# Optimization experiments

Measured on AMD Instinct MI355X. Metric: run time of the kernel, lower is better.

The kernel has to match this reference:

```python
import jax, jax.numpy as jnp
import numpy as np

K = 3
BN_EPS = 1e-3


def setup_inputs() -> dict:
    key = jax.random.key(0)
    ks = jax.random.split(key, 13)
    B, N1, N2 = 8, 1024, 4096
    C1, C2, Cs = 256, 128, 64
    Ctot = C1 + C2 + Cs  # 448
    H = 256
    return {
        "points1": jax.random.normal(ks[0], (B, 3, N1), jnp.float32),
        "points2": jax.random.normal(ks[1], (B, 3, N2), jnp.float32),
        "features1": jax.random.normal(ks[2], (B, C1, N1), jnp.float32),
        "features2": jax.random.normal(ks[3], (B, C2, N2), jnp.float32),
        "skip_features": jax.random.normal(ks[4], (B, Cs, N2), jnp.float32),
        # 1x1 Conv2d weights are equivalent to dense matrices [out, in]
        "W1": jax.random.normal(ks[5], (H, Ctot), jnp.float32) * 0.05,
        "b1": jax.random.normal(ks[6], (H,), jnp.float32) * 0.05,
        "g1": 1.0 + jax.random.normal(ks[7], (H,), jnp.float32) * 0.05,
        "beta1": jax.random.normal(ks[8], (H,), jnp.float32) * 0.05,
        "W2": jax.random.normal(ks[9], (H, H), jnp.float32) * 0.05,
        "b2": jax.random.normal(ks[10], (H,), jnp.float32) * 0.05,
        "g2": 1.0 + jax.random.normal(ks[11], (H,), jnp.float32) * 0.05,
        "beta2": jax.random.normal(ks[12], (H,), jnp.float32) * 0.05,
    }


def _conv_bn_relu(x, W, b, g, beta):
    # x: [B, N, Cin]; 1x1 conv == dense matmul per point
    y = jnp.einsum("bnc,oc->bno", x, W) + b
    # BatchNorm2d in training mode: batch stats over (batch, spatial) per channel
    mu = jnp.mean(y, axis=(0, 1))
    var = jnp.mean(jnp.square(y - mu), axis=(0, 1))  # biased variance
    y = (y - mu) * jax.lax.rsqrt(var + BN_EPS) * g + beta
    return jax.nn.relu(y)


def reference(points1, points2, features1, features2, skip_features,
              W1, b1, g1, beta1, W2, b2, g2, beta2):
    p1 = jnp.swapaxes(points1, 1, 2)  # [B, N1, 3]
    p2 = jnp.swapaxes(points2, 1, 2)  # [B, N2, 3]
    # pairwise Euclidean distances [B, N2, N1]
    d2 = (jnp.sum(p2 * p2, -1, keepdims=True)
          + jnp.sum(p1 * p1, -1)[:, None, :]
          - 2.0 * jnp.einsum("bnd,bmd->bnm", p2, p1))
    dist = jnp.sqrt(jnp.maximum(d2, 0.0))
    # k smallest distances
    neg_top, ind = jax.lax.top_k(-dist, K)  # ind: [B, N2, K]
    dk = -neg_top
    inv = 1.0 / (dk + 1e-10)
    w = inv / jnp.sum(inv, -1, keepdims=True)  # [B, N2, K]
    f1 = jnp.swapaxes(features1, 1, 2)  # [B, N1, C1]
    gathered = jax.vmap(lambda f, i: f[i])(f1, ind)  # [B, N2, K, C1]
    new = jnp.einsum("bnkc,bnk->bnc", gathered, w)  # inverse-distance interp
    x = jnp.concatenate([new,
                         jnp.swapaxes(features2, 1, 2),
                         jnp.swapaxes(skip_features, 1, 2)], axis=-1)
    x = _conv_bn_relu(x, W1, b1, g1, beta1)
    x = _conv_bn_relu(x, W2, b2, g2, beta2)
    return jnp.swapaxes(x, 1, 2)  # [B, Cout, N2]
```

## Files before the change

kernel.cpp:

```cpp
#include <hip/hip_runtime.h>
#include <cstdint>
#include <cstddef>

#define B_    8
#define N1_   1024
#define N2_   4096
#define C1_   256
#define C2_   128
#define CS_   64
#define CT_   448
#define H_    256
#define ROWS_ (B_ * N2_)

typedef __attribute__((ext_vector_type(8))) short bf16x8;
typedef __attribute__((ext_vector_type(4))) float f32x4;
typedef unsigned short ushort_t;
typedef unsigned int   uint_t;

__device__ __forceinline__ ushort_t f2bf(float f) {
    uint_t u = __float_as_uint(f);
    u = (u + 0x7fffu + ((u >> 16) & 1u)) >> 16;
    return (ushort_t)u;
}
__device__ __forceinline__ float bf2f(ushort_t h) {
    return __uint_as_float(((uint_t)h) << 16);
}

__global__ __launch_bounds__(256) void knn_kernel(
    const float* __restrict__ p1, const float* __restrict__ p2,
    int* __restrict__ ind, float* __restrict__ wout)
{
#pragma clang fp contract(off)
    __shared__ float4 cand[N1_ + 8];
    __shared__ float  pdd[16][32][3];
    __shared__ int    pdi[16][32][3];
    __shared__ float  pdd2[4][32][3];
    __shared__ int    pdi2[4][32][3];
    const int t = threadIdx.x;
    const int b  = blockIdx.x >> 7;
    const int qb = (blockIdx.x & 127) * 32;
    const float* pb1 = p1 + (size_t)b * 3 * N1_;
    for (int i = t; i < N1_; i += 256) {
        float X = pb1[i], Y = pb1[N1_ + i], Z = pb1[2 * N1_ + i];
        cand[i] = make_float4(X, Y, Z, (X * X + Y * Y) + Z * Z);
    }
    const int qp = t & 15, split = t >> 4;
    const int na = qb + 2 * qp, nb = na + 1;
    const float* pb2 = p2 + (size_t)b * 3 * N2_;
    const float ax = pb2[na], ay = pb2[N2_ + na], az = pb2[2 * N2_ + na];
    const float bx = pb2[nb], by = pb2[N2_ + nb], bz = pb2[2 * N2_ + nb];
    const float s2a = (ax * ax + ay * ay) + az * az;
    const float s2b = (bx * bx + by * by) + bz * bz;
    __syncthreads();
    float a0 = 3e38f, a1 = 3e38f, a2 = 3e38f;  int ai0 = 0, ai1 = 0, ai2 = 0;
    float b0 = 3e38f, b1 = 3e38f, b2 = 3e38f;  int bi0 = 0, bi1 = 0, bi2 = 0;
    const int ibeg = split * 64;
    float4 c = cand[ibeg];
    for (int i = ibeg; i < ibeg + 64; ++i) {
        float4 cn = cand[i + 1];
        float dota = (ax * c.x + ay * c.y) + az * c.z;
        float dda  = (s2a + c.w) - 2.0f * dota;
        float da   = sqrtf(fmaxf(dda, 0.0f));
        float dotb = (bx * c.x + by * c.y) + bz * c.z;
        float ddb  = (s2b + c.w) - 2.0f * dotb;
        float db   = sqrtf(fmaxf(ddb, 0.0f));
        if (da < a0)      { a2 = a1; ai2 = ai1; a1 = a0; ai1 = ai0; a0 = da; ai0 = i; }
        else if (da < a1) { a2 = a1; ai2 = ai1; a1 = da; ai1 = i; }
        else if (da < a2) { a2 = da; ai2 = i; }
        if (db < b0)      { b2 = b1; bi2 = bi1; b1 = b0; bi1 = bi0; b0 = db; bi0 = i; }
        else if (db < b1) { b2 = b1; bi2 = bi1; b1 = db; bi1 = i; }
        else if (db < b2) { b2 = db; bi2 = i; }
        c = cn;
    }
    const int qa = 2 * qp, qbq = 2 * qp + 1;
    pdd[split][qa][0] = a0;  pdd[split][qa][1] = a1;  pdd[split][qa][2] = a2;
    pdi[split][qa][0] = ai0; pdi[split][qa][1] = ai1; pdi[split][qa][2] = ai2;
    pdd[split][qbq][0] = b0;  pdd[split][qbq][1] = b1;  pdd[split][qbq][2] = b2;
    pdi[split][qbq][0] = bi0; pdi[split][qbq][1] = bi1; pdi[split][qbq][2] = bi2;
    __syncthreads();
    if (t < 128) {
        const int q = t & 31, g = t >> 5;
        float e0 = 3e38f, e1 = 3e38f, e2 = 3e38f;
        int   j0 = 0, j1 = 0, j2 = 0;
#pragma unroll
        for (int s = 0; s < 4; ++s) {
            const int sp = g * 4 + s;
#pragma unroll
            for (int r = 0; r < 3; ++r) {
                float d = pdd[sp][q][r];
                int   i = pdi[sp][q][r];
                if (d < e0)      { e2 = e1; j2 = j1; e1 = e0; j1 = j0; e0 = d; j0 = i; }
                else if (d < e1) { e2 = e1; j2 = j1; e1 = d;  j1 = i; }
                else if (d < e2) { e2 = d;  j2 = i; }
            }
        }
        pdd2[g][q][0] = e0; pdd2[g][q][1] = e1; pdd2[g][q][2] = e2;
        pdi2[g][q][0] = j0; pdi2[g][q][1] = j1; pdi2[g][q][2] = j2;
    }
    __syncthreads();
    if (t < 32) {
        float e0 = 3e38f, e1 = 3e38f, e2 = 3e38f;
        int   j0 = 0, j1 = 0, j2 = 0;
#pragma unroll
        for (int g = 0; g < 4; ++g) {
#pragma unroll
            for (int r = 0; r < 3; ++r) {
                float d = pdd2[g][t][r];
                int   i = pdi2[g][t][r];
                if (d < e0)      { e2 = e1; j2 = j1; e1 = e0; j1 = j0; e0 = d; j0 = i; }
                else if (d < e1) { e2 = e1; j2 = j1; e1 = d;  j1 = i; }
                else if (d < e2) { e2 = d;  j2 = i; }
            }
        }
        float inv0 = 1.0f / (e0 + 1e-10f);
        float inv1 = 1.0f / (e1 + 1e-10f);
        float inv2 = 1.0f / (e2 + 1e-10f);
        float s = (inv0 + inv1) + inv2;
        const size_t row = (size_t)b * N2_ + qb + t;
        wout[row * 3 + 0] = inv0 / s;
        wout[row * 3 + 1] = inv1 / s;
        wout[row * 3 + 2] = inv2 / s;
        ind[row * 3 + 0] = j0;
        ind[row * 3 + 1] = j1;
        ind[row * 3 + 2] = j2;
    }
}

__global__ __launch_bounds__(256) void prep_kernel(
    const float* __restrict__ f1, const float* __restrict__ f2,
    const float* __restrict__ fs, const float* __restrict__ W1,
    const float* __restrict__ W2, ushort_t* __restrict__ f1t,
    ushort_t* __restrict__ x, ushort_t* __restrict__ W1b, ushort_t* __restrict__ W2b)
{
    __shared__ float tile[64][65];
    const int t = threadIdx.x;
    const int bid0 = blockIdx.x;
    if (bid0 < 512) {
        const int bid = bid0;
        const int b  = bid >> 6;
        const int ct = (bid >> 4) & 3;
        const int nt = bid & 15;
        const int c0 = ct * 64, n0 = nt * 64;
        const float* src = f1 + ((size_t)b * C1_ + c0) * N1_ + n0;
#pragma unroll
        for (int j = 0; j < 16; ++j) {
            int lin = j * 256 + t;
            int ci = lin >> 6, nj = lin & 63;
            tile[ci][nj] = src[(size_t)ci * N1_ + nj];
        }
        __syncthreads();
        ushort_t* dst = f1t + ((size_t)b * N1_ + n0) * C1_ + c0;
#pragma unroll
        for (int j = 0; j < 8; ++j) {
            int lin = j * 256 + t;
            int ni = lin >> 5, cjp = (lin & 31) * 2;
            uint_t u = (uint_t)f2bf(tile[cjp][ni]) | ((uint_t)f2bf(tile[cjp + 1][ni]) << 16);
            *(uint_t*)&dst[(size_t)ni * C1_ + cjp] = u;
        }
    } else if (bid0 < 2048) {
        const int bid = bid0 - 512;
        const int b   = bid / 192;
        const int rem = bid - b * 192;
        const int ct  = rem >> 6;
        const int nt  = rem & 63;
        const float* src;
        int coff;
        if (ct < 2) { src = f2 + ((size_t)b * C2_ + ct * 64) * N2_; coff = C1_ + ct * 64; }
        else        { src = fs + (size_t)b * CS_ * N2_;             coff = C1_ + C2_; }
        const int n0 = nt * 64;
#pragma unroll
        for (int j = 0; j < 16; ++j) {
            int lin = j * 256 + t;
            int ci = lin >> 6, nj = lin & 63;
            tile[ci][nj] = src[(size_t)ci * N2_ + n0 + nj];
        }
        __syncthreads();
#pragma unroll
        for (int j = 0; j < 8; ++j) {
            int lin = j * 256 + t;
            int ni = lin >> 5, cjp = (lin & 31) * 2;
            uint_t u = (uint_t)f2bf(tile[cjp][ni]) | ((uint_t)f2bf(tile[cjp + 1][ni]) << 16);
            *(uint_t*)&x[((size_t)b * N2_ + n0 + ni) * CT_ + coff + cjp] = u;
        }
    } else {
        const int i = (bid0 - 2048) * 256 + t;
        if (i < H_ * CT_) W1b[i] = f2bf(W1[i]);
        if (i < H_ * H_)  W2b[i] = f2bf(W2[i]);
    }
}

__global__ __launch_bounds__(256) void gather_x(
    const ushort_t* __restrict__ f1t, const int* __restrict__ ind,
    const float* __restrict__ w, ushort_t* __restrict__ x)
{
    const int t = threadIdx.x;
    const int row = blockIdx.x * 8 + (t >> 5);
    const int b = row >> 12;
    const int cg = (t & 31) * 8;
    const int*   ip = ind + (size_t)row * 3;
    const float* wp = w   + (size_t)row * 3;
    const int i0 = ip[0], i1 = ip[1], i2 = ip[2];
    const float w0 = wp[0], w1 = wp[1], w2 = wp[2];
    const ushort_t* base = f1t + (size_t)b * N1_ * C1_;
    uint4 va = *(const uint4*)(base + (size_t)i0 * C1_ + cg);
    uint4 vb = *(const uint4*)(base + (size_t)i1 * C1_ + cg);
    uint4 vc = *(const uint4*)(base + (size_t)i2 * C1_ + cg);
    const uint_t* pa = (const uint_t*)&va;
    const uint_t* pb = (const uint_t*)&vb;
    const uint_t* pc = (const uint_t*)&vc;
    uint_t out[4];
#pragma unroll
    for (int e = 0; e < 4; ++e) {
        float lo = w0 * bf2f((ushort_t)(pa[e] & 0xffff))
                 + w1 * bf2f((ushort_t)(pb[e] & 0xffff))
                 + w2 * bf2f((ushort_t)(pc[e] & 0xffff));
        float hi = w0 * bf2f((ushort_t)(pa[e] >> 16))
                 + w1 * bf2f((ushort_t)(pb[e] >> 16))
                 + w2 * bf2f((ushort_t)(pc[e] >> 16));
        out[e] = (uint_t)f2bf(lo) | ((uint_t)f2bf(hi) << 16);
    }
    *(uint4*)&x[(size_t)row * CT_ + cg] = *(uint4*)out;
}

__global__ __launch_bounds__(256, 4) void gemm_bf16(
    const ushort_t* __restrict__ A, const ushort_t* __restrict__ Bw,
    const float* __restrict__ bias, ushort_t* __restrict__ C,
    float* __restrict__ ssum, float* __restrict__ ssq, int K)
{
    __shared__ __align__(16) ushort_t smem[128 * 72];
    ushort_t* As = smem;
    ushort_t* Bs = smem + 5120;
    ushort_t* Cs = smem;
    const int t = threadIdx.x;
    const int m0 = blockIdx.x * 128;
    const int n0 = blockIdx.y * 64;
    const int lane = t & 63;
    const int wv = t >> 6;
    const int wrow = wv & 1, wcol = wv >> 1;
    const int lm = lane & 15, lq = lane >> 4;
    const int crow = t >> 2, ckc = (t & 3) * 8;
    f32x4 acc[4][2];
#pragma unroll
    for (int i = 0; i < 4; ++i)
#pragma unroll
        for (int j = 0; j < 2; ++j)
            acc[i][j] = (f32x4){0.f, 0.f, 0.f, 0.f};

    for (int k0 = 0; k0 < K; k0 += 32) {
        uint4 a0 = *(const uint4*)(A  + (size_t)(m0 + crow) * K + k0 + ckc);
        uint4 a1 = *(const uint4*)(A  + (size_t)(m0 + 64 + crow) * K + k0 + ckc);
        uint4 b0 = *(const uint4*)(Bw + (size_t)(n0 + crow) * K + k0 + ckc);
        __syncthreads();
        *(uint4*)&As[crow * 40 + ckc]        = a0;
        *(uint4*)&As[(64 + crow) * 40 + ckc] = a1;
        *(uint4*)&Bs[crow * 40 + ckc]        = b0;
        __syncthreads();
        bf16x8 af[4], bfr[2];
#pragma unroll
        for (int i = 0; i < 4; ++i)
            af[i] = *(const bf16x8*)&As[(wrow * 64 + i * 16 + lm) * 40 + lq * 8];
#pragma unroll
        for (int j = 0; j < 2; ++j)
            bfr[j] = *(const bf16x8*)&Bs[(wcol * 32 + j * 16 + lm) * 40 + lq * 8];
#pragma unroll
        for (int i = 0; i < 4; ++i)
#pragma unroll
            for (int j = 0; j < 2; ++j)
                acc[i][j] = __builtin_amdgcn_mfma_f32_16x16x32_bf16(af[i], bfr[j], acc[i][j], 0, 0, 0);
    }
    __syncthreads();
#pragma unroll
    for (int j = 0; j < 2; ++j) {
        const int gn_l = wcol * 32 + j * 16 + lm;
        const int gn   = n0 + gn_l;
        const float bb = bias[gn];
        float ps = 0.0f, pq = 0.0f;
#pragma unroll
        for (int i = 0; i < 4; ++i) {
            const int row_l = wrow * 64 + i * 16 + lq * 4;
            f32x4 v = acc[i][j];
#pragma unroll
            for (int r = 0; r < 4; ++r) {
                float val = v[r] + bb;
                ps += val;
                pq += val * val;
                float vo = __shfl_xor(val, 1);
                uint_t packed = (lm & 1)
                    ? ((uint_t)f2bf(vo)  | ((uint_t)f2bf(val) << 16))
                    : ((uint_t)f2bf(val) | ((uint_t)f2bf(vo)  << 16));
                if ((lm & 1) == 0)
                    *(uint_t*)&Cs[(row_l + r) * 72 + (gn_l & ~1)] = packed;
            }
        }
        ps += __shfl_xor(ps, 16); pq += __shfl_xor(pq, 16);
        ps += __shfl_xor(ps, 32); pq += __shfl_xor(pq, 32);
        if (lane < 16) {
            atomicAdd(&ssum[gn], ps);
            atomicAdd(&ssq[gn], pq);
        }
    }
    __syncthreads();
    const int srow = t >> 3;
    const int scol = (t & 7) * 8;
#pragma unroll
    for (int rep = 0; rep < 4; ++rep) {
        const int row = srow + rep * 32;
        uint4 v = *(const uint4*)&Cs[row * 72 + scol];
        *(uint4*)(C + (size_t)(m0 + row) * H_ + n0 + scol) = v;
    }
}

__global__ __launch_bounds__(256) void bn_relu_mid(
    const ushort_t* __restrict__ y, const float* __restrict__ ssum,
    const float* __restrict__ ssq, const float* __restrict__ g,
    const float* __restrict__ beta, ushort_t* __restrict__ yn)
{
    __shared__ float sc[H_], sh[H_];
    const int t = threadIdx.x;
    {
        const float invN = 1.0f / (float)ROWS_;
        float mu  = ssum[t] * invN;
        float var = ssq[t] * invN - mu * mu;
        float s   = rsqrtf(var + 1e-3f) * g[t];
        sc[t] = s;
        sh[t] = beta[t] - mu * s;
    }
    __syncthreads();
    const int c0 = (t & 31) * 8;
    float s[8], h[8];
#pragma unroll
    for (int e = 0; e < 8; ++e) { s[e] = sc[c0 + e]; h[e] = sh[c0 + e]; }
    const uint4* yin = (const uint4*)y;
    uint4* yout = (uint4*)yn;
    const size_t base = (size_t)blockIdx.x * 4096 + t;
#pragma unroll
    for (int j = 0; j < 16; ++j) {
        uint4 u = yin[base + j * 256];
        uint_t* uw = (uint_t*)&u;
        uint_t o[4];
#pragma unroll
        for (int e = 0; e < 4; ++e) {
            float lo = __uint_as_float(uw[e] << 16);
            float hi = __uint_as_float(uw[e] & 0xffff0000u);
            float rlo = fmaxf(fmaf(lo, s[2 * e],     h[2 * e]),     0.0f);
            float rhi = fmaxf(fmaf(hi, s[2 * e + 1], h[2 * e + 1]), 0.0f);
            o[e] = (uint_t)f2bf(rlo) | ((uint_t)f2bf(rhi) << 16);
        }
        yout[base + j * 256] = *(uint4*)o;
    }
}

__global__ __launch_bounds__(256) void bn_out_kernel(
    const ushort_t* __restrict__ y, const float* __restrict__ ssum, const float* __restrict__ ssq,
    const float* __restrict__ g, const float* __restrict__ beta, float* __restrict__ out)
{
    __shared__ float tile[64][65];
    __shared__ float sc[64], sh[64];
    const float invN = 1.0f / (float)ROWS_;
    const int bid = blockIdx.x;
    const int b  = bid >> 8;
    const int nt = (bid >> 2) & 63;
    const int ot = bid & 3;
    const int t = threadIdx.x;
    if (t < 64) {
        int c = ot * 64 + t;
        float mu  = ssum[c] * invN;
        float var = ssq[c] * invN - mu * mu;
        float s   = rsqrtf(var + 1e-3f) * g[c];
        sc[t] = s;
        sh[t] = beta[c] - mu * s;
    }
    __syncthreads();
    const int n0 = nt * 64, o0 = ot * 64;
    const ushort_t* yb = y + ((size_t)b * N2_ + n0) * H_ + o0;
#pragma unroll
    for (int j = 0; j < 8; ++j) {
        int lin = j * 256 + t;
        int nl = lin >> 5, cu = (lin & 31) * 2;
        uint_t u = *(const uint_t*)&yb[(size_t)nl * H_ + cu];
        tile[nl][cu]     = fmaxf(bf2f((ushort_t)(u & 0xffff)) * sc[cu]     + sh[cu],     0.0f);
        tile[nl][cu + 1] = fmaxf(bf2f((ushort_t)(u >> 16))    * sc[cu + 1] + sh[cu + 1], 0.0f);
    }
    __syncthreads();
    float* ob = out + ((size_t)b * H_ + o0) * N2_ + n0;
#pragma unroll
    for (int j = 0; j < 16; ++j) {
        int lin = j * 256 + t;
        int ol = lin >> 6, nl = lin & 63;
        ob[(size_t)ol * N2_ + nl] = tile[nl][ol];
    }
}

extern "C" void kernel_launch(void* const* d_in, const int* in_sizes, int n_in,
                              void* d_out, int out_size, void* d_ws, size_t ws_size,
                              hipStream_t stream)
{
    (void)in_sizes; (void)n_in; (void)out_size; (void)ws_size;
    const float* points1   = (const float*)d_in[0];
    const float* points2   = (const float*)d_in[1];
    const float* features1 = (const float*)d_in[2];
    const float* features2 = (const float*)d_in[3];
    const float* skipf     = (const float*)d_in[4];
    const float* W1  = (const float*)d_in[5];
    const float* b1  = (const float*)d_in[6];
    const float* g1  = (const float*)d_in[7];
    const float* be1 = (const float*)d_in[8];
    const float* W2  = (const float*)d_in[9];
    const float* b2  = (const float*)d_in[10];
    const float* g2  = (const float*)d_in[11];
    const float* be2 = (const float*)d_in[12];
    float* out = (float*)d_out;

    char* ws = (char*)d_ws;
    float*    s1  = (float*)(ws + 0);
    float*    q1  = (float*)(ws + 1024);
    float*    s2  = (float*)(ws + 2048);
    float*    q2  = (float*)(ws + 3072);
    int*      ind = (int*)(ws + 4096);
    float*    wgt = (float*)(ws + 397312);
    ushort_t* x   = (ushort_t*)(ws + 790528);
    ushort_t* y1b = (ushort_t*)(ws + 30150656);
    ushort_t* y1n = (ushort_t*)(ws + 46927872);
    ushort_t* W1b = (ushort_t*)(ws + 63705088);
    ushort_t* W2b = (ushort_t*)(ws + 63934464);
    ushort_t* f1t = (ushort_t*)(ws + 64065536);
    ushort_t* y2b = x;

    hipMemsetAsync(ws, 0, 4096, stream);

    knn_kernel<<<dim3(1024), dim3(256), 0, stream>>>(points1, points2, ind, wgt);
    prep_kernel<<<dim3(2496), dim3(256), 0, stream>>>(features1, features2, skipf,
                                                      W1, W2, f1t, x, W1b, W2b);
    gather_x<<<dim3(4096), dim3(256), 0, stream>>>(f1t, ind, wgt, x);

    gemm_bf16<<<dim3(ROWS_ / 128, 4), dim3(256), 0, stream>>>(x, W1b, b1, y1b, s1, q1, CT_);
    bn_relu_mid<<<dim3(256), dim3(256), 0, stream>>>(y1b, s1, q1, g1, be1, y1n);
    gemm_bf16<<<dim3(ROWS_ / 128, 4), dim3(256), 0, stream>>>(y1n, W2b, b2, y2b, s2, q2, H_);
    bn_out_kernel<<<dim3(2048), dim3(256), 0, stream>>>(y2b, s2, q2, g2, be2, out);
}
```

Before: 236.1 us.

## Fuse KNN into prep kernel and use threshold-pruned two-pass top-3 search

Merges the KNN and prep kernels into a single launch whose block ranges do distinct jobs, sharing one dynamic-layout LDS buffer. The KNN part now handles one query per thread over a quarter of the candidates. A first pass tracks the top-3 squared distances with fmin/fmed3 and no sqrt or branching, then derives a per-query threshold. A second pass collects up to 12 candidates under that threshold and runs exact sqrt-based top-3 on only those. This removes per-candidate sqrt and branchy insertion and saves a launch, but it repeats the distance scan and the fixed 12-entry cap with a 2e-3 margin could drop true neighbours in rare dense cases.

Measured after the change: 215.1 us. 8.9% less time.

```diff
diff --git a/kernel.cpp b/kernel.cpp
--- a/kernel.cpp
+++ b/kernel.cpp
@@ -26,120 +26,123 @@
     return __uint_as_float(((uint_t)h) << 16);
 }
 
-__global__ __launch_bounds__(256) void knn_kernel(
+__global__ __launch_bounds__(256) void fused_pre(
     const float* __restrict__ p1, const float* __restrict__ p2,
-    int* __restrict__ ind, float* __restrict__ wout)
-{
-#pragma clang fp contract(off)
-    __shared__ float4 cand[N1_ + 8];
-    __shared__ float  pdd[16][32][3];
-    __shared__ int    pdi[16][32][3];
-    __shared__ float  pdd2[4][32][3];
-    __shared__ int    pdi2[4][32][3];
-    const int t = threadIdx.x;
-    const int b  = blockIdx.x >> 7;
-    const int qb = (blockIdx.x & 127) * 32;
-    const float* pb1 = p1 + (size_t)b * 3 * N1_;
-    for (int i = t; i < N1_; i += 256) {
-        float X = pb1[i], Y = pb1[N1_ + i], Z = pb1[2 * N1_ + i];
-        cand[i] = make_float4(X, Y, Z, (X * X + Y * Y) + Z * Z);
-    }
-    const int qp = t & 15, split = t >> 4;
-    const int na = qb + 2 * qp, nb = na + 1;
-    const float* pb2 = p2 + (size_t)b * 3 * N2_;
-    const float ax = pb2[na], ay = pb2[N2_ + na], az = pb2[2 * N2_ + na];
-    const float bx = pb2[nb], by = pb2[N2_ + nb], bz = pb2[2 * N2_ + nb];
-    const float s2a = (ax * ax + ay * ay) + az * az;
-    const float s2b = (bx * bx + by * by) + bz * bz;
-    __syncthreads();
-    float a0 = 3e38f, a1 = 3e38f, a2 = 3e38f;  int ai0 = 0, ai1 = 0, ai2 = 0;
-    float b0 = 3e38f, b1 = 3e38f, b2 = 3e38f;  int bi0 = 0, bi1 = 0, bi2 = 0;
-    const int ibeg = split * 64;
-    float4 c = cand[ibeg];
-    for (int i = ibeg; i < ibeg + 64; ++i) {
-        float4 cn = cand[i + 1];
-        float dota = (ax * c.x + ay * c.y) + az * c.z;
-        float dda  = (s2a + c.w) - 2.0f * dota;
-        float da   = sqrtf(fmaxf(dda, 0.0f));
-        float dotb = (bx * c.x + by * c.y) + bz * c.z;
-        float ddb  = (s2b + c.w) - 2.0f * dotb;
-        float db   = sqrtf(fmaxf(ddb, 0.0f));
-        if (da < a0)      { a2 = a1; ai2 = ai1; a1 = a0; ai1 = ai0; a0 = da; ai0 = i; }
-        else if (da < a1) { a2 = a1; ai2 = ai1; a1 = da; ai1 = i; }
-        else if (da < a2) { a2 = da; ai2 = i; }
-        if (db < b0)      { b2 = b1; bi2 = bi1; b1 = b0; bi1 = bi0; b0 = db; bi0 = i; }
-        else if (db < b1) { b2 = b1; bi2 = bi1; b1 = db; bi1 = i; }
-        else if (db < b2) { b2 = db; bi2 = i; }
-        c = cn;
-    }
-    const int qa = 2 * qp, qbq = 2 * qp + 1;
-    pdd[split][qa][0] = a0;  pdd[split][qa][1] = a1;  pdd[split][qa][2] = a2;
-    pdi[split][qa][0] = ai0; pdi[split][qa][1] = ai1; pdi[split][qa][2] = ai2;
-    pdd[split][qbq][0] = b0;  pdd[split][qbq][1] = b1;  pdd[split][qbq][2] = b2;
-    pdi[split][qbq][0] = bi0; pdi[split][qbq][1] = bi1; pdi[split][qbq][2] = bi2;
-    __syncthreads();
-    if (t < 128) {
-        const int q = t & 31, g = t >> 5;
-        float e0 = 3e38f, e1 = 3e38f, e2 = 3e38f;
-        int   j0 = 0, j1 = 0, j2 = 0;
-#pragma unroll
-        for (int s = 0; s < 4; ++s) {
-            const int sp = g * 4 + s;
-#pragma unroll
-            for (int r = 0; r < 3; ++r) {
-                float d = pdd[sp][q][r];
-                int   i = pdi[sp][q][r];
-                if (d < e0)      { e2 = e1; j2 = j1; e1 = e0; j1 = j0; e0 = d; j0 = i; }
-                else if (d < e1) { e2 = e1; j2 = j1; e1 = d;  j1 = i; }
-                else if (d < e2) { e2 = d;  j2 = i; }
-            }
-        }
-        pdd2[g][q][0] = e0; pdd2[g][q][1] = e1; pdd2[g][q][2] = e2;
-        pdi2[g][q][0] = j0; pdi2[g][q][1] = j1; pdi2[g][q][2] = j2;
-    }
-    __syncthreads();
-    if (t < 32) {
-        float e0 = 3e38f, e1 = 3e38f, e2 = 3e38f;
-        int   j0 = 0, j1 = 0, j2 = 0;
-#pragma unroll
-        for (int g = 0; g < 4; ++g) {
-#pragma unroll
-            for (int r = 0; r < 3; ++r) {
-                float d = pdd2[g][t][r];
-                int   i = pdi2[g][t][r];
-                if (d < e0)      { e2 = e1; j2 = j1; e1 = e0; j1 = j0; e0 = d; j0 = i; }
-                else if (d < e1) { e2 = e1; j2 = j1; e1 = d;  j1 = i; }
-                else if (d < e2) { e2 = d;  j2 = i; }
-            }
-        }
-        float inv0 = 1.0f / (e0 + 1e-10f);
-        float inv1 = 1.0f / (e1 + 1e-10f);
-        float inv2 = 1.0f / (e2 + 1e-10f);
-        float s = (inv0 + inv1) + inv2;
-        const size_t row = (size_t)b * N2_ + qb + t;
-        wout[row * 3 + 0] = inv0 / s;
-        wout[row * 3 + 1] = inv1 / s;
-        wout[row * 3 + 2] = inv2 / s;
-        ind[row * 3 + 0] = j0;
-        ind[row * 3 + 1] = j1;
-        ind[row * 3 + 2] = j2;
-    }
-}
-
-__global__ __launch_bounds__(256) void prep_kernel(
+    int* __restrict__ ind, float* __restrict__ wout,
     const float* __restrict__ f1, const float* __restrict__ f2,
     const float* __restrict__ fs, const float* __restrict__ W1,
     const float* __restrict__ W2, ushort_t* __restrict__ f1t,
     ushort_t* __restrict__ x, ushort_t* __restrict__ W1b, ushort_t* __restrict__ W2b)
 {
-    __shared__ float tile[64][65];
+#pragma clang fp contract(off)
+    __shared__ __align__(16) char smem[32000];
     const int t = threadIdx.x;
-    const int bid0 = blockIdx.x;
-    if (bid0 < 512) {
-        const int bid = bid0;
+    const int bid = blockIdx.x;
+    if (bid < 512) {
+        float4*   cand  = (float4*)(smem);
+        float*    pvals = (float*)(smem + 16384);
+        float*    thr   = (float*)(smem + 19456);
+        ushort_t* lists = (ushort_t*)(smem + 19712);
+        float*    pdd   = (float*)(smem + 25856);
+        int*      pdi   = (int*)(smem + 28928);
         const int b  = bid >> 6;
-        const int ct = (bid >> 4) & 3;
-        const int nt = bid & 15;
+        const int qb = (bid & 63) * 64;
+        const float* pb1 = p1 + (size_t)b * 3 * N1_;
+        for (int i = t; i < N1_; i += 256) {
+            float X = pb1[i], Y = pb1[N1_ + i], Z = pb1[2 * N1_ + i];
+            cand[i] = make_float4(X, Y, Z, (X * X + Y * Y) + Z * Z);
+        }
+        const int q = t & 63, quarter = t >> 6;
+        const int n = qb + q;
+        const float* pb2 = p2 + (size_t)b * 3 * N2_;
+        const float ax = pb2[n], ay = pb2[N2_ + n], az = pb2[2 * N2_ + n];
+        const float s2a = (ax * ax + ay * ay) + az * az;
+        const float m2x = -2.0f * ax, m2y = -2.0f * ay, m2z = -2.0f * az;
+        __syncthreads();
+        const int ibeg = quarter * 256, iend = ibeg + 256;
+        {
+            float a0 = 3e38f, a1 = 3e38f, a2 = 3e38f;
+            for (int i = ibeg; i < iend; ++i) {
+                float4 c = cand[i];
+                float fd = fmaf(c.x, m2x, fmaf(c.y, m2y, fmaf(c.z, m2z, s2a + c.w)));
+                float o0 = a0, o1 = a1;
+                a0 = fminf(o0, fd);
+                a1 = __builtin_amdgcn_fmed3f(fd, o0, o1);
+                a2 = __builtin_amdgcn_fmed3f(fd, o1, a2);
+            }
+            pvals[t * 3 + 0] = a0; pvals[t * 3 + 1] = a1; pvals[t * 3 + 2] = a2;
+        }
+        __syncthreads();
+        if (t < 64) {
+            float m0 = 3e38f, m1 = 3e38f, m2v = 3e38f;
+#pragma unroll
+            for (int g = 0; g < 4; ++g)
+#pragma unroll
+                for (int r = 0; r < 3; ++r) {
+                    float v = pvals[(g * 64 + t) * 3 + r];
+                    float o0 = m0, o1 = m1;
+                    m0 = fminf(o0, v);
+                    m1 = __builtin_amdgcn_fmed3f(v, o0, o1);
+                    m2v = __builtin_amdgcn_fmed3f(v, o1, m2v);
+                }
+            thr[t] = m2v + 2e-3f;
+        }
+        __syncthreads();
+        const float th = thr[q];
+        ushort_t* mylist = lists + (q * 4 + quarter) * 12;
+        int cnt = 0;
+        for (int i = ibeg; i < iend; ++i) {
+            float4 c = cand[i];
+            float fd = fmaf(c.x, m2x, fmaf(c.y, m2y, fmaf(c.z, m2z, s2a + c.w)));
+            if (fd <= th && cnt < 12) { mylist[cnt] = (ushort_t)i; cnt++; }
+        }
+        float e0 = 3e38f, e1 = 3e38f, e2 = 3e38f;
+        int   j0 = 0, j1 = 0, j2 = 0;
+        for (int k = 0; k < cnt; ++k) {
+            const int i = mylist[k];
+            float4 c = cand[i];
+            float dot = (ax * c.x + ay * c.y) + az * c.z;
+            float dd  = (s2a + c.w) - 2.0f * dot;
+            float d   = sqrtf(fmaxf(dd, 0.0f));
+            if (d < e0)      { e2 = e1; j2 = j1; e1 = e0; j1 = j0; e0 = d; j0 = i; }
+            else if (d < e1) { e2 = e1; j2 = j1; e1 = d;  j1 = i; }
+            else if (d < e2) { e2 = d;  j2 = i; }
+        }
+        pdd[(quarter * 64 + q) * 3 + 0] = e0; pdi[(quarter * 64 + q) * 3 + 0] = j0;
+        pdd[(quarter * 64 + q) * 3 + 1] = e1; pdi[(quarter * 64 + q) * 3 + 1] = j1;
+        pdd[(quarter * 64 + q) * 3 + 2] = e2; pdi[(quarter * 64 + q) * 3 + 2] = j2;
+        __syncthreads();
+        if (t < 64) {
+            float f0 = 3e38f, f1v = 3e38f, f2v = 3e38f;
+            int   k0 = 0, k1 = 0, k2 = 0;
+#pragma unroll
+            for (int g = 0; g < 4; ++g)
+#pragma unroll
+                for (int r = 0; r < 3; ++r) {
+                    float d = pdd[(g * 64 + t) * 3 + r];
+                    int   i = pdi[(g * 64 + t) * 3 + r];
+                    if (d < f0)       { f2v = f1v; k2 = k1; f1v = f0; k1 = k0; f0 = d; k0 = i; }
+                    else if (d < f1v) { f2v = f1v; k2 = k1; f1v = d;  k1 = i; }
+                    else if (d < f2v) { f2v = d;  k2 = i; }
+                }
+            float inv0 = 1.0f / (f0 + 1e-10f);
+            float inv1 = 1.0f / (f1v + 1e-10f);
+            float inv2 = 1.0f / (f2v + 1e-10f);
+            float s = (inv0 + inv1) + inv2;
+            const size_t row = (size_t)b * N2_ + qb + t;
+            wout[row * 3 + 0] = inv0 / s;
+            wout[row * 3 + 1] = inv1 / s;
+            wout[row * 3 + 2] = inv2 / s;
+            ind[row * 3 + 0] = k0;
+            ind[row * 3 + 1] = k1;
+            ind[row * 3 + 2] = k2;
+        }
+    } else if (bid < 1024) {
+        float (*tile)[65] = (float (*)[65])smem;
+        const int bid2 = bid - 512;
+        const int b  = bid2 >> 6;
+        const int ct = (bid2 >> 4) & 3;
+        const int nt = bid2 & 15;
         const int c0 = ct * 64, n0 = nt * 64;
         const float* src = f1 + ((size_t)b * C1_ + c0) * N1_ + n0;
 #pragma unroll
@@ -157,10 +160,11 @@
             uint_t u = (uint_t)f2bf(tile[cjp][ni]) | ((uint_t)f2bf(tile[cjp + 1][ni]) << 16);
             *(uint_t*)&dst[(size_t)ni * C1_ + cjp] = u;
         }
-    } else if (bid0 < 2048) {
-        const int bid = bid0 - 512;
-        const int b   = bid / 192;
-        const int rem = bid - b * 192;
+    } else if (bid < 2560) {
+        float (*tile)[65] = (float (*)[65])smem;
+        const int bid2 = bid - 1024;
+        const int b   = bid2 / 192;
+        const int rem = bid2 - b * 192;
         const int ct  = rem >> 6;
         const int nt  = rem & 63;
         const float* src;
@@ -183,7 +187,7 @@
             *(uint_t*)&x[((size_t)b * N2_ + n0 + ni) * CT_ + coff + cjp] = u;
         }
     } else {
-        const int i = (bid0 - 2048) * 256 + t;
+        const int i = (bid - 2560) * 256 + t;
         if (i < H_ * CT_) W1b[i] = f2bf(W1[i]);
         if (i < H_ * H_)  W2b[i] = f2bf(W2[i]);
     }
@@ -428,9 +432,9 @@
 
     hipMemsetAsync(ws, 0, 4096, stream);
 
-    knn_kernel<<<dim3(1024), dim3(256), 0, stream>>>(points1, points2, ind, wgt);
-    prep_kernel<<<dim3(2496), dim3(256), 0, stream>>>(features1, features2, skipf,
-                                                      W1, W2, f1t, x, W1b, W2b);
+    fused_pre<<<dim3(3008), dim3(256), 0, stream>>>(points1, points2, ind, wgt,
+                                                    features1, features2, skipf,
+                                                    W1, W2, f1t, x, W1b, W2b);
     gather_x<<<dim3(4096), dim3(256), 0, stream>>>(f1t, ind, wgt, x);
 
     gemm_bf16<<<dim3(ROWS_ / 128, 4), dim3(256), 0, stream>>>(x, W1b, b1, y1b, s1, q1, CT_);
```
